# Kernel optimization log

Hardware: AMD Instinct MI355X
Metric: run time of the kernel (lower is better)

Reference implementation:

```python
import jax, jax.numpy as jnp
import numpy as np
from jax import lax

C = 768
SHIFT_DISTANCES = (1, 2, 3)


def _layernorm(x, g, b, eps=1e-5):
    m = jnp.mean(x, axis=-1, keepdims=True)
    v = jnp.mean((x - m) ** 2, axis=-1, keepdims=True)
    return (x - m) * lax.rsqrt(v + eps) * g + b


def setup_inputs() -> dict:
    key = jax.random.key(0)
    ks = jax.random.split(key, 16)
    B, T, N = 8, 16, 197
    inp = {
        "x": jax.random.normal(ks[0], (B * T, N, C), dtype=jnp.float32),
        "ln_g": jnp.ones((C,), jnp.float32),
        "ln_b": jnp.zeros((C,), jnp.float32),
        "gate_w": jax.random.normal(ks[1], (C, C), jnp.float32) * 0.02,
        "gate_b": jnp.zeros((C,), jnp.float32),
        "proj_w1": jax.random.normal(ks[2], (C, C), jnp.float32) * 0.02,
        "proj_b1": jnp.zeros((C,), jnp.float32),
        "proj_w2": jax.random.normal(ks[3], (C, C), jnp.float32) * 0.02,
        "proj_b2": jnp.zeros((C,), jnp.float32),
        "fusion_w": jnp.ones((len(SHIFT_DISTANCES),), jnp.float32),
        "num_frames": T,
    }
    for i, d in enumerate(SHIFT_DISTANCES):
        k = 2 * d + 1
        # depthwise Conv1d weight: (out=C, in/groups=1, k)
        inp[f"conv_w{i}"] = jax.random.normal(ks[4 + i], (C, 1, k), jnp.float32) * (1.0 / np.sqrt(k))
        inp[f"conv_b{i}"] = jnp.zeros((C,), jnp.float32)
    return inp


def _branch(x4, conv_w, conv_b, d, ln_g, ln_b, gate_w, gate_b):
    # x4: [B, T, N, C]
    B, T, N, Cc = x4.shape
    p = Cc // 3  # past / future split; static gets the remainder
    x_norm = jax.nn.relu(_layernorm(x4, ln_g, ln_b))
    # [B, T, N, C] -> [B*N, C, T] for depthwise conv over time
    x_1d = x_norm.transpose(0, 2, 3, 1).reshape(B * N, Cc, T)
    feat = lax.conv_general_dilated(
        x_1d, conv_w, window_strides=(1,), padding=[(d, d)],
        dimension_numbers=("NCH", "OIH", "NCH"), feature_group_count=Cc,
    ) + conv_b[None, :, None]
    feat = feat.reshape(B, N, Cc, T).transpose(0, 3, 1, 2)  # [B, T, N, C]
    gate = jax.nn.sigmoid(jnp.einsum("btnc,cd->btnd", feat, gate_w) + gate_b)
    y = gate * x4  # channelwise split-and-multiply fuses into one op
    y_past, y_future, y_static = y[..., :p], y[..., p:2 * p], y[..., 2 * p:]
    s = min(d, T)
    out_past = jnp.pad(y_past[:, s:], ((0, 0), (0, s), (0, 0), (0, 0)))  # lshift
    out_future = jnp.pad(y_future[:, :T - s], ((0, 0), (s, 0), (0, 0), (0, 0)))  # rshift
    return jnp.concatenate([out_past, out_future, y_static], axis=-1)


def reference(x, ln_g, ln_b, gate_w, gate_b, proj_w1, proj_b1, proj_w2, proj_b2,
              fusion_w, conv_w0, conv_b0, conv_w1, conv_b1, conv_w2, conv_b2,
              num_frames):
    B_T, N, Cc = x.shape
    T = num_frames
    B = B_T // T
    x4 = x.reshape(B, T, N, Cc)
    convs = [(conv_w0, conv_b0), (conv_w1, conv_b1), (conv_w2, conv_b2)]
    outs = jnp.stack([
        _branch(x4, cw, cb, d, ln_g, ln_b, gate_w, gate_b)
        for (cw, cb), d in zip(convs, SHIFT_DISTANCES)
    ], axis=0)  # [3, B, T, N, C]
    w = jax.nn.softmax(fusion_w)[:, None, None, None, None]
    fused = jnp.sum(w * outs, axis=0).reshape(B_T, N, Cc)
    h = jnp.einsum("bnc,cd->bnd", fused, proj_w1) + proj_b1
    h = jax.nn.gelu(h, approximate=False)
    h = jnp.einsum("bnc,cd->bnd", h, proj_w2) + proj_b2
    return x + h
```

## Files before the change

kernel.cpp:

```cpp
#include <hip/hip_runtime.h>
#include <math.h>


#define MROWS 25216
#define CD    768
#define NTOK  197
#define TFR   16

typedef __attribute__((ext_vector_type(8))) short short8;
typedef __attribute__((ext_vector_type(4))) float floatx4;
typedef unsigned int u32;

__device__ __forceinline__ unsigned short f2bf(float f) {
    union { float f; unsigned u; } v; v.f = f;
    unsigned r = v.u + 0x7FFFu + ((v.u >> 16) & 1u);
    return (unsigned short)(r >> 16);
}
__device__ __forceinline__ float bf2f(unsigned short h) {
    union { unsigned u; float f; } v; v.u = ((unsigned)h) << 16;
    return v.f;
}

__device__ __forceinline__ void gl2lds16(const void* g, void* l) {
    __builtin_amdgcn_global_load_lds(
        (__attribute__((address_space(1))) void*)(unsigned long long)g,
        (__attribute__((address_space(3))) void*)(u32)(unsigned long long)l,
        16, 0, 0);
}

__global__ __launch_bounds__(256)
void ln_relu_kernel(const float* __restrict__ x, const float* __restrict__ g,
                    const float* __restrict__ b, unsigned short* __restrict__ xn,
                    unsigned short* __restrict__ xb) {
    int row = blockIdx.x;
    int tid = threadIdx.x;
    const float* xr = x + (size_t)row * CD;
    float v0 = xr[tid], v1 = xr[tid + 256], v2 = xr[tid + 512];
    float s = v0 + v1 + v2;
    __shared__ float red[8];
#pragma unroll
    for (int off = 32; off; off >>= 1) s += __shfl_down(s, off, 64);
    int lane = tid & 63, w = tid >> 6;
    if (lane == 0) red[w] = s;
    __syncthreads();
    float mean = (red[0] + red[1] + red[2] + red[3]) * (1.0f / CD);
    float d0 = v0 - mean, d1 = v1 - mean, d2 = v2 - mean;
    float s2 = d0 * d0 + d1 * d1 + d2 * d2;
#pragma unroll
    for (int off = 32; off; off >>= 1) s2 += __shfl_down(s2, off, 64);
    if (lane == 0) red[4 + w] = s2;
    __syncthreads();
    float var = (red[4] + red[5] + red[6] + red[7]) * (1.0f / CD);
    float inv = rsqrtf(var + 1e-5f);
    unsigned short* xo = xn + (size_t)row * CD;
    unsigned short* xc = xb + (size_t)row * CD;
    float o0 = fmaxf(d0 * inv * g[tid]       + b[tid],       0.0f);
    float o1 = fmaxf(d1 * inv * g[tid + 256] + b[tid + 256], 0.0f);
    float o2 = fmaxf(d2 * inv * g[tid + 512] + b[tid + 512], 0.0f);
    xo[tid] = f2bf(o0); xo[tid + 256] = f2bf(o1); xo[tid + 512] = f2bf(o2);
    xc[tid] = f2bf(v0); xc[tid + 256] = f2bf(v1); xc[tid + 512] = f2bf(v2);
}

template <int D>
__device__ __forceinline__
void dw_body(const unsigned short* __restrict__ xn, const float* __restrict__ cw,
             const float* __restrict__ cb, unsigned short* __restrict__ feat) {
    constexpr int KK = 2 * D + 1;
    int gid = blockIdx.x * 256 + threadIdx.x;
    int bn = gid / 96;
    int cg = gid - bn * 96;
    int c0 = cg * 8;
    int b = bn / NTOK;
    size_t base = ((size_t)b * TFR * NTOK + (bn - b * NTOK)) * CD + c0;
    const size_t tstride = (size_t)NTOK * CD;

    short8 u[TFR];
#pragma unroll
    for (int t = 0; t < TFR; ++t)
        u[t] = *(const short8*)(xn + base + (size_t)t * tstride);

    float wgt[8][KK], bb[8];
#pragma unroll
    for (int q = 0; q < 8; ++q) {
        bb[q] = cb[c0 + q];
#pragma unroll
        for (int j = 0; j < KK; ++j) wgt[q][j] = cw[(c0 + q) * KK + j];
    }

#pragma unroll
    for (int t = 0; t < TFR; ++t) {
        float acc[8];
#pragma unroll
        for (int q = 0; q < 8; ++q) acc[q] = bb[q];
#pragma unroll
        for (int j = 0; j < KK; ++j) {
            int tj = t + j - D;
            if (tj < 0 || tj >= TFR) continue;
#pragma unroll
            for (int q = 0; q < 8; ++q)
                acc[q] += bf2f((unsigned short)u[tj][q]) * wgt[q][j];
        }
        short8 o;
#pragma unroll
        for (int q = 0; q < 8; ++q) o[q] = (short)f2bf(acc[q]);
        *(short8*)(feat + base + (size_t)t * tstride) = o;
    }
}

__global__ __launch_bounds__(256)
void dwconv_all(const unsigned short* __restrict__ xn,
                const float* __restrict__ cw0, const float* __restrict__ cb0,
                const float* __restrict__ cw1, const float* __restrict__ cb1,
                const float* __restrict__ cw2, const float* __restrict__ cb2,
                unsigned short* __restrict__ f1, unsigned short* __restrict__ f2,
                unsigned short* __restrict__ f3) {
    if (blockIdx.y == 0)      dw_body<1>(xn, cw0, cb0, f1);
    else if (blockIdx.y == 1) dw_body<2>(xn, cw1, cb1, f2);
    else                      dw_body<3>(xn, cw2, cb2, f3);
}

__global__ __launch_bounds__(256)
void wprep3_kernel(const float* __restrict__ w0, const float* __restrict__ w1,
                   const float* __restrict__ w2, unsigned short* __restrict__ t0,
                   unsigned short* __restrict__ t1, unsigned short* __restrict__ t2) {
    const float* w = blockIdx.y == 0 ? w0 : blockIdx.y == 1 ? w1 : w2;
    unsigned short* wt = blockIdx.y == 0 ? t0 : blockIdx.y == 1 ? t1 : t2;
    int gid = blockIdx.x * 256 + threadIdx.x;
    int n = gid / CD, k = gid - n * CD;
    wt[gid] = f2bf(w[(size_t)k * CD + n]);
}

__global__ __launch_bounds__(256)
void fuse_kernel(const unsigned short* __restrict__ y1,
                 const unsigned short* __restrict__ y2,
                 const unsigned short* __restrict__ y3,
                 unsigned short* __restrict__ fused) {
    int gid = blockIdx.x * 256 + threadIdx.x;
    int m = gid / 96;
    int kk = (gid - m * 96) * 8;
    int t = (m / NTOK) & 15;
    float vals[8] = {0.f, 0.f, 0.f, 0.f, 0.f, 0.f, 0.f, 0.f};
    const unsigned short* ys[3] = {y1, y2, y3};
#pragma unroll
    for (int d = 1; d <= 3; ++d) {
        int src; bool ok;
        if (kk < 256)      { src = m + d * NTOK; ok = (t + d) < TFR; }
        else if (kk < 512) { src = m - d * NTOK; ok = (t - d) >= 0; }
        else               { src = m;            ok = true; }
        if (ok) {
            short8 u = *(const short8*)(ys[d - 1] + (size_t)src * CD + kk);
#pragma unroll
            for (int e = 0; e < 8; ++e) vals[e] += bf2f((unsigned short)u[e]);
        }
    }
    short8 o;
#pragma unroll
    for (int e = 0; e < 8; ++e) o[e] = (short)f2bf(vals[e]);
    *(short8*)(fused + (size_t)m * CD + kk) = o;
}

template <int EPI>
__global__ __launch_bounds__(512)
void gemm_kernel(const unsigned short* __restrict__ A,
                 const unsigned short* __restrict__ Bt,
                 const float* __restrict__ bias,
                 const unsigned short* __restrict__ xb,
                 const float* __restrict__ xf,
                 float* __restrict__ outf,
                 unsigned short* __restrict__ outh0,
                 unsigned short* __restrict__ outh1,
                 unsigned short* __restrict__ outh2,
                 const float* __restrict__ fw) {
    extern __shared__ __align__(16) char smem[];
    int tid  = threadIdx.x;
    int m0   = blockIdx.x * 128;
    int n0   = blockIdx.y * 256;
    int wave = tid >> 6, lane = tid & 63;
    int wr   = wave >> 2, wc = wave & 3;
    int quad = lane >> 4, l16 = lane & 15;
    int rr   = lane >> 3;
    int ckx  = ((lane & 7) ^ rr) * 8;

    floatx4 acc[4][4];
#pragma unroll
    for (int i = 0; i < 4; ++i)
#pragma unroll
        for (int j = 0; j < 4; ++j) acc[i][j] = (floatx4){0.f, 0.f, 0.f, 0.f};

    auto Asb = [&](int bb) { return (unsigned short*)(smem + bb * 16384); };
    auto Bsb = [&](int bb) { return (unsigned short*)(smem + 49152 + bb * 32768); };

    auto sA = [&](int t, int bb, int h) {
        int q = wave + h * 8;
        gl2lds16(A + (size_t)(m0 + q * 8 + rr) * CD + t * 64 + ckx, Asb(bb) + q * 512);
    };
    auto sB = [&](int t, int bb, int h) {
        int q = wave + h * 8;
        gl2lds16(Bt + (size_t)(n0 + q * 8 + rr) * CD + t * 64 + ckx, Bsb(bb) + q * 512);
    };
    auto ldA = [&](int bb, int i, int kk) -> short8 {
        int r = wr * 64 + i * 16 + l16;
        int slot = (kk * 4 + quad) ^ (l16 & 7);
        return *(const short8*)((const char*)Asb(bb) + r * 128 + slot * 16);
    };
    auto ldB = [&](int bb, int j, int kk) -> short8 {
        int r = wc * 64 + j * 16 + l16;
        int slot = (kk * 4 + quad) ^ (l16 & 7);
        return *(const short8*)((const char*)Bsb(bb) + r * 128 + slot * 16);
    };

#define LGKM0 do { asm volatile("s_waitcnt lgkmcnt(0)" ::: "memory"); \
                   __builtin_amdgcn_sched_barrier(0); } while (0)
#define PBAR  do { __builtin_amdgcn_s_barrier(); \
                   __builtin_amdgcn_sched_barrier(0); } while (0)

    auto kstep = [&](int t, bool doStage) {
        int bb = t % 3, bn = (t + 2) % 3;
        short8 a0[4], a1[4], u, v;
#pragma unroll
        for (int i = 0; i < 4; ++i) a0[i] = ldA(bb, i, 0);
        u = ldB(bb, 0, 0); v = ldB(bb, 1, 0);
        if (doStage) { sA(t + 2, bn, 0); sA(t + 2, bn, 1); }
        LGKM0;
        __builtin_amdgcn_s_setprio(1);
#pragma unroll
        for (int i = 0; i < 4; ++i) {
            acc[i][0] = __builtin_amdgcn_mfma_f32_16x16x32_bf16(a0[i], u, acc[i][0], 0, 0, 0);
            acc[i][1] = __builtin_amdgcn_mfma_f32_16x16x32_bf16(a0[i], v, acc[i][1], 0, 0, 0);
        }
        __builtin_amdgcn_s_setprio(0);
        PBAR;
        u = ldB(bb, 2, 0); v = ldB(bb, 3, 0);
        if (doStage) { sB(t + 2, bn, 0); sB(t + 2, bn, 1); }
        LGKM0;
        __builtin_amdgcn_s_setprio(1);
#pragma unroll
        for (int i = 0; i < 4; ++i) {
            acc[i][2] = __builtin_amdgcn_mfma_f32_16x16x32_bf16(a0[i], u, acc[i][2], 0, 0, 0);
            acc[i][3] = __builtin_amdgcn_mfma_f32_16x16x32_bf16(a0[i], v, acc[i][3], 0, 0, 0);
        }
        __builtin_amdgcn_s_setprio(0);
        PBAR;
#pragma unroll
        for (int i = 0; i < 4; ++i) a1[i] = ldA(bb, i, 1);
        u = ldB(bb, 0, 1); v = ldB(bb, 1, 1);
        if (doStage) { sB(t + 2, bn, 2); sB(t + 2, bn, 3); }
        LGKM0;
        __builtin_amdgcn_s_setprio(1);
#pragma unroll
        for (int i = 0; i < 4; ++i) {
            acc[i][0] = __builtin_amdgcn_mfma_f32_16x16x32_bf16(a1[i], u, acc[i][0], 0, 0, 0);
            acc[i][1] = __builtin_amdgcn_mfma_f32_16x16x32_bf16(a1[i], v, acc[i][1], 0, 0, 0);
        }
        __builtin_amdgcn_s_setprio(0);
        PBAR;
        u = ldB(bb, 2, 1); v = ldB(bb, 3, 1);
        LGKM0;
        __builtin_amdgcn_s_setprio(1);
#pragma unroll
        for (int i = 0; i < 4; ++i) {
            acc[i][2] = __builtin_amdgcn_mfma_f32_16x16x32_bf16(a1[i], u, acc[i][2], 0, 0, 0);
            acc[i][3] = __builtin_amdgcn_mfma_f32_16x16x32_bf16(a1[i], v, acc[i][3], 0, 0, 0);
        }
        __builtin_amdgcn_s_setprio(0);
    };

    constexpr int NT = CD / 64;
    sA(0, 0, 0); sA(0, 0, 1); sB(0, 0, 0); sB(0, 0, 1); sB(0, 0, 2); sB(0, 0, 3);
    sA(1, 1, 0); sA(1, 1, 1); sB(1, 1, 0); sB(1, 1, 1); sB(1, 1, 2); sB(1, 1, 3);
    for (int t = 0; t < NT - 1; ++t) {
        asm volatile("s_waitcnt vmcnt(6)" ::: "memory");
        PBAR;
        kstep(t, t + 2 < NT);
    }
    asm volatile("s_waitcnt vmcnt(0)" ::: "memory");
    PBAR;
    kstep(NT - 1, false);

    float wd = 0.f;
    int widx = (EPI == 0) ? (blockIdx.x / 197) : 0;
    unsigned short* outh = outh0;
    if (EPI == 0) {
        float f0 = fw[0], f1 = fw[1], f2 = fw[2];
        float mx = fmaxf(f0, fmaxf(f1, f2));
        float e0 = expf(f0 - mx), e1 = expf(f1 - mx), e2 = expf(f2 - mx);
        float inv = 1.f / (e0 + e1 + e2);
        wd = (widx == 0 ? e0 : widx == 1 ? e1 : e2) * inv;
        outh = widx == 0 ? outh0 : widx == 1 ? outh1 : outh2;
    }

    float (*fE)[268] = (float (*)[268])smem;
    __syncthreads();
#pragma unroll
    for (int j = 0; j < 4; ++j) {
        int col = wc * 64 + j * 16 + l16;
        float bc = bias[n0 + col];
#pragma unroll
        for (int i = 0; i < 4; ++i)
#pragma unroll
            for (int r = 0; r < 4; ++r)
                fE[wr * 64 + i * 16 + quad * 4 + r][col] = acc[i][j][r] + bc;
    }
    __syncthreads();
#pragma unroll
    for (int it = 0; it < 8; ++it) {
        int lr = it * 16 + (tid >> 5);
        int cg = tid & 31;
        size_t lrow = (size_t)(m0 + lr) - (size_t)widx * MROWS;
        int gcol = n0 + cg * 8;
        size_t idx = lrow * CD + gcol;
        floatx4 v0 = *(const floatx4*)&fE[lr][cg * 8];
        floatx4 v1 = *(const floatx4*)&fE[lr][cg * 8 + 4];
        if (EPI == 0) {
            short8 xv = *(const short8*)(xb + idx);
            short8 o;
#pragma unroll
            for (int e = 0; e < 8; ++e) {
                float vv = e < 4 ? v0[e] : v1[e - 4];
                float gte = 1.f / (1.f + expf(-vv));
                o[e] = (short)f2bf(wd * gte * bf2f((unsigned short)xv[e]));
            }
            *(short8*)(outh + idx) = o;
        } else if (EPI == 1) {
            short8 o;
#pragma unroll
            for (int e = 0; e < 8; ++e) {
                float vv = e < 4 ? v0[e] : v1[e - 4];
                float gl = 0.5f * vv * (1.0f + erff(vv * 0.70710678118f));
                o[e] = (short)f2bf(gl);
            }
            *(short8*)(outh + idx) = o;
        } else {
            floatx4 x0 = *(const floatx4*)(xf + idx);
            floatx4 x1 = *(const floatx4*)(xf + idx + 4);
#pragma unroll
            for (int e = 0; e < 4; ++e) { v0[e] += x0[e]; v1[e] += x1[e]; }
            *(floatx4*)(outf + idx)     = v0;
            *(floatx4*)(outf + idx + 4) = v1;
        }
    }
#undef LGKM0
#undef PBAR
}

extern "C" void kernel_launch(void* const* d_in, const int* in_sizes, int n_in,
                              void* d_out, int out_size, void* d_ws, size_t ws_size,
                              hipStream_t stream) {
    const float* x      = (const float*)d_in[0];
    const float* ln_g   = (const float*)d_in[1];
    const float* ln_b   = (const float*)d_in[2];
    const float* gate_w = (const float*)d_in[3];
    const float* gate_b = (const float*)d_in[4];
    const float* pw1    = (const float*)d_in[5];
    const float* pb1    = (const float*)d_in[6];
    const float* pw2    = (const float*)d_in[7];
    const float* pb2    = (const float*)d_in[8];
    const float* fw     = (const float*)d_in[9];
    const float* cw[3]  = {(const float*)d_in[11], (const float*)d_in[13], (const float*)d_in[15]};
    const float* cb[3]  = {(const float*)d_in[12], (const float*)d_in[14], (const float*)d_in[16]};

    char* ws = (char*)d_ws;
    const size_t SB = (size_t)MROWS * CD * 2;
    unsigned short* gwt  = (unsigned short*)(ws + 0);
    unsigned short* p1t  = (unsigned short*)(ws + 1179648);
    unsigned short* p2t  = (unsigned short*)(ws + 2359296);
    unsigned short* xn   = (unsigned short*)(ws + 3538944);
    unsigned short* xb   = (unsigned short*)(ws + 3538944 + SB);
    unsigned short* f1   = (unsigned short*)(ws + 3538944 + 2 * SB);
    unsigned short* f2   = (unsigned short*)(ws + 3538944 + 3 * SB);
    unsigned short* f3   = (unsigned short*)(ws + 3538944 + 4 * SB);
    unsigned short* y2s  = (unsigned short*)(ws + 3538944 + 5 * SB);
    unsigned short* y3s  = (unsigned short*)(ws + 3538944 + 6 * SB);
    unsigned short* y1    = xn;
    unsigned short* fused = f3;
    unsigned short* h1    = xn;

    const int LDSB = 147456;
    hipFuncSetAttribute(reinterpret_cast<const void*>(gemm_kernel<0>),
                        hipFuncAttributeMaxDynamicSharedMemorySize, LDSB);
    hipFuncSetAttribute(reinterpret_cast<const void*>(gemm_kernel<1>),
                        hipFuncAttributeMaxDynamicSharedMemorySize, LDSB);
    hipFuncSetAttribute(reinterpret_cast<const void*>(gemm_kernel<2>),
                        hipFuncAttributeMaxDynamicSharedMemorySize, LDSB);

    dim3 wg(2304, 3);
    wprep3_kernel<<<wg, 256, 0, stream>>>(gate_w, pw1, pw2, gwt, p1t, p2t);
    ln_relu_kernel<<<MROWS, 256, 0, stream>>>(x, ln_g, ln_b, xn, xb);

    dim3 dg(591, 3);
    dwconv_all<<<dg, 256, 0, stream>>>(xn, cw[0], cb[0], cw[1], cb[1], cw[2], cb[2],
                                       f1, f2, f3);

    dim3 gg3(591, 3);
    gemm_kernel<0><<<gg3, 512, LDSB, stream>>>(f1, gwt, gate_b, xb, nullptr,
                                               nullptr, y1, y2s, y3s, fw);

    fuse_kernel<<<9456, 256, 0, stream>>>(y1, y2s, y3s, fused);

    dim3 gg(197, 3);
    gemm_kernel<1><<<gg, 512, LDSB, stream>>>(fused, p1t, pb1, nullptr, nullptr,
                                              nullptr, h1, nullptr, nullptr, nullptr);
    gemm_kernel<2><<<gg, 512, LDSB, stream>>>(h1, p2t, pb2, nullptr, x,
                                              (float*)d_out, nullptr, nullptr, nullptr, nullptr);
}
```

Measured before the change: 529.2 us.

## Fuse layernorm into depthwise conv and shrink GEMM K-tile for higher occupancy

Merges the layernorm+ReLU kernel with the three depthwise temporal convolutions, so each block handles one (batch, token) column across all frames. This removes the bf16 normalized intermediate and its extra global round trip. The GEMM K-step drops from 64 to 32, cutting LDS from 147KB to 72KB with a new swizzle, and launch bounds now request more resident blocks. The epilogue is staged in two halves to fit the smaller LDS, and expf is swapped for __expf. The tradeoffs are more K iterations and barriers in the GEMM and only 192 threads per conv block.

```diff
diff --git a/kernel.cpp b/kernel.cpp
--- a/kernel.cpp
+++ b/kernel.cpp
@@ -8,6 +8,7 @@
 #define TFR   16
 
 typedef __attribute__((ext_vector_type(8))) short short8;
+typedef __attribute__((ext_vector_type(4))) short short4v;
 typedef __attribute__((ext_vector_type(4))) float floatx4;
 typedef unsigned int u32;
 
@@ -28,95 +29,105 @@
         16, 0, 0);
 }
 
-__global__ __launch_bounds__(256)
-void ln_relu_kernel(const float* __restrict__ x, const float* __restrict__ g,
-                    const float* __restrict__ b, unsigned short* __restrict__ xn,
-                    unsigned short* __restrict__ xb) {
-    int row = blockIdx.x;
-    int tid = threadIdx.x;
-    const float* xr = x + (size_t)row * CD;
-    float v0 = xr[tid], v1 = xr[tid + 256], v2 = xr[tid + 512];
-    float s = v0 + v1 + v2;
-    __shared__ float red[8];
-#pragma unroll
-    for (int off = 32; off; off >>= 1) s += __shfl_down(s, off, 64);
-    int lane = tid & 63, w = tid >> 6;
-    if (lane == 0) red[w] = s;
-    __syncthreads();
-    float mean = (red[0] + red[1] + red[2] + red[3]) * (1.0f / CD);
-    float d0 = v0 - mean, d1 = v1 - mean, d2 = v2 - mean;
-    float s2 = d0 * d0 + d1 * d1 + d2 * d2;
-#pragma unroll
-    for (int off = 32; off; off >>= 1) s2 += __shfl_down(s2, off, 64);
-    if (lane == 0) red[4 + w] = s2;
-    __syncthreads();
-    float var = (red[4] + red[5] + red[6] + red[7]) * (1.0f / CD);
-    float inv = rsqrtf(var + 1e-5f);
-    unsigned short* xo = xn + (size_t)row * CD;
-    unsigned short* xc = xb + (size_t)row * CD;
-    float o0 = fmaxf(d0 * inv * g[tid]       + b[tid],       0.0f);
-    float o1 = fmaxf(d1 * inv * g[tid + 256] + b[tid + 256], 0.0f);
-    float o2 = fmaxf(d2 * inv * g[tid + 512] + b[tid + 512], 0.0f);
-    xo[tid] = f2bf(o0); xo[tid + 256] = f2bf(o1); xo[tid + 512] = f2bf(o2);
-    xc[tid] = f2bf(v0); xc[tid + 256] = f2bf(v1); xc[tid + 512] = f2bf(v2);
-}
-
 template <int D>
 __device__ __forceinline__
-void dw_body(const unsigned short* __restrict__ xn, const float* __restrict__ cw,
-             const float* __restrict__ cb, unsigned short* __restrict__ feat) {
+void dw_store(const float (&xn)[TFR][4], const float* __restrict__ cw,
+              const float* __restrict__ cb, unsigned short* __restrict__ f,
+              size_t base, size_t tstr, int c0) {
     constexpr int KK = 2 * D + 1;
-    int gid = blockIdx.x * 256 + threadIdx.x;
-    int bn = gid / 96;
-    int cg = gid - bn * 96;
-    int c0 = cg * 8;
-    int b = bn / NTOK;
-    size_t base = ((size_t)b * TFR * NTOK + (bn - b * NTOK)) * CD + c0;
-    const size_t tstride = (size_t)NTOK * CD;
-
-    short8 u[TFR];
-#pragma unroll
-    for (int t = 0; t < TFR; ++t)
-        u[t] = *(const short8*)(xn + base + (size_t)t * tstride);
-
-    float wgt[8][KK], bb[8];
-#pragma unroll
-    for (int q = 0; q < 8; ++q) {
-        bb[q] = cb[c0 + q];
-#pragma unroll
-        for (int j = 0; j < KK; ++j) wgt[q][j] = cw[(c0 + q) * KK + j];
-    }
-
-#pragma unroll
-    for (int t = 0; t < TFR; ++t) {
-        float acc[8];
-#pragma unroll
-        for (int q = 0; q < 8; ++q) acc[q] = bb[q];
+    float wj[4][KK], cbv[4];
+#pragma unroll
+    for (int q = 0; q < 4; ++q) {
+        cbv[q] = cb[c0 + q];
+#pragma unroll
+        for (int j = 0; j < KK; ++j) wj[q][j] = cw[(c0 + q) * KK + j];
+    }
+#pragma unroll
+    for (int t = 0; t < TFR; ++t) {
+        float acc[4] = {cbv[0], cbv[1], cbv[2], cbv[3]};
 #pragma unroll
         for (int j = 0; j < KK; ++j) {
             int tj = t + j - D;
             if (tj < 0 || tj >= TFR) continue;
 #pragma unroll
-            for (int q = 0; q < 8; ++q)
-                acc[q] += bf2f((unsigned short)u[tj][q]) * wgt[q][j];
-        }
-        short8 o;
-#pragma unroll
-        for (int q = 0; q < 8; ++q) o[q] = (short)f2bf(acc[q]);
-        *(short8*)(feat + base + (size_t)t * tstride) = o;
-    }
-}
-
-__global__ __launch_bounds__(256)
-void dwconv_all(const unsigned short* __restrict__ xn,
-                const float* __restrict__ cw0, const float* __restrict__ cb0,
-                const float* __restrict__ cw1, const float* __restrict__ cb1,
-                const float* __restrict__ cw2, const float* __restrict__ cb2,
-                unsigned short* __restrict__ f1, unsigned short* __restrict__ f2,
-                unsigned short* __restrict__ f3) {
-    if (blockIdx.y == 0)      dw_body<1>(xn, cw0, cb0, f1);
-    else if (blockIdx.y == 1) dw_body<2>(xn, cw1, cb1, f2);
-    else                      dw_body<3>(xn, cw2, cb2, f3);
+            for (int q = 0; q < 4; ++q) acc[q] += xn[tj][q] * wj[q][j];
+        }
+        short4v o;
+#pragma unroll
+        for (int q = 0; q < 4; ++q) o[q] = (short)f2bf(acc[q]);
+        *(short4v*)(f + base + t * tstr) = o;
+    }
+}
+
+__global__ __launch_bounds__(192)
+void ln_dw_kernel(const float* __restrict__ x, const float* __restrict__ g,
+                  const float* __restrict__ bia,
+                  const float* __restrict__ cw0, const float* __restrict__ cb0,
+                  const float* __restrict__ cw1, const float* __restrict__ cb1,
+                  const float* __restrict__ cw2, const float* __restrict__ cb2,
+                  unsigned short* __restrict__ xb,
+                  unsigned short* __restrict__ f1,
+                  unsigned short* __restrict__ f2,
+                  unsigned short* __restrict__ f3) {
+    int blk = blockIdx.x, tid = threadIdx.x;
+    int b = blk / NTOK, n = blk - b * NTOK;
+    int c0 = tid * 4;
+    size_t base = ((size_t)b * TFR * NTOK + n) * CD + c0;
+    const size_t tstr = (size_t)NTOK * CD;
+    int lane = tid & 63, w = tid >> 6;
+
+    float xn[TFR][4];
+    float ps[TFR];
+#pragma unroll
+    for (int t = 0; t < TFR; ++t) {
+        float4 xv = *(const float4*)(x + base + t * tstr);
+        xn[t][0] = xv.x; xn[t][1] = xv.y; xn[t][2] = xv.z; xn[t][3] = xv.w;
+        ps[t] = xv.x + xv.y + xv.z + xv.w;
+        short4v o; o[0] = (short)f2bf(xv.x); o[1] = (short)f2bf(xv.y);
+        o[2] = (short)f2bf(xv.z); o[3] = (short)f2bf(xv.w);
+        *(short4v*)(xb + base + t * tstr) = o;
+    }
+    __shared__ float red[TFR][4];
+#pragma unroll
+    for (int t = 0; t < TFR; ++t) {
+        float v = ps[t];
+#pragma unroll
+        for (int off = 32; off; off >>= 1) v += __shfl_down(v, off, 64);
+        if (lane == 0) red[t][w] = v;
+    }
+    __syncthreads();
+    float mean[TFR];
+#pragma unroll
+    for (int t = 0; t < TFR; ++t) mean[t] = (red[t][0] + red[t][1] + red[t][2]) * (1.0f / CD);
+    __syncthreads();
+#pragma unroll
+    for (int t = 0; t < TFR; ++t) {
+        float d0 = xn[t][0] - mean[t], d1 = xn[t][1] - mean[t];
+        float d2 = xn[t][2] - mean[t], d3 = xn[t][3] - mean[t];
+        ps[t] = d0 * d0 + d1 * d1 + d2 * d2 + d3 * d3;
+    }
+#pragma unroll
+    for (int t = 0; t < TFR; ++t) {
+        float v = ps[t];
+#pragma unroll
+        for (int off = 32; off; off >>= 1) v += __shfl_down(v, off, 64);
+        if (lane == 0) red[t][w] = v;
+    }
+    __syncthreads();
+    float gv[4], bv[4];
+#pragma unroll
+    for (int q = 0; q < 4; ++q) { gv[q] = g[c0 + q]; bv[q] = bia[c0 + q]; }
+#pragma unroll
+    for (int t = 0; t < TFR; ++t) {
+        float var = (red[t][0] + red[t][1] + red[t][2]) * (1.0f / CD);
+        float inv = rsqrtf(var + 1e-5f);
+#pragma unroll
+        for (int q = 0; q < 4; ++q)
+            xn[t][q] = fmaxf((xn[t][q] - mean[t]) * inv * gv[q] + bv[q], 0.0f);
+    }
+    dw_store<1>(xn, cw0, cb0, f1, base, tstr, c0);
+    dw_store<2>(xn, cw1, cb1, f2, base, tstr, c0);
+    dw_store<3>(xn, cw2, cb2, f3, base, tstr, c0);
 }
 
 __global__ __launch_bounds__(256)
@@ -160,7 +171,7 @@
 }
 
 template <int EPI>
-__global__ __launch_bounds__(512)
+__global__ __launch_bounds__(512, 4)
 void gemm_kernel(const unsigned short* __restrict__ A,
                  const unsigned short* __restrict__ Bt,
                  const float* __restrict__ bias,
@@ -178,8 +189,9 @@
     int wave = tid >> 6, lane = tid & 63;
     int wr   = wave >> 2, wc = wave & 3;
     int quad = lane >> 4, l16 = lane & 15;
-    int rr   = lane >> 3;
-    int ckx  = ((lane & 7) ^ rr) * 8;
+    int r4   = lane >> 2;
+    int ckx  = (((lane & 3) ^ ((lane >> 3) & 3)) * 8);
+    int rdsl = (quad ^ ((l16 >> 1) & 3)) * 16;
 
     floatx4 acc[4][4];
 #pragma unroll
@@ -187,26 +199,22 @@
 #pragma unroll
         for (int j = 0; j < 4; ++j) acc[i][j] = (floatx4){0.f, 0.f, 0.f, 0.f};
 
-    auto Asb = [&](int bb) { return (unsigned short*)(smem + bb * 16384); };
-    auto Bsb = [&](int bb) { return (unsigned short*)(smem + 49152 + bb * 32768); };
-
-    auto sA = [&](int t, int bb, int h) {
-        int q = wave + h * 8;
-        gl2lds16(A + (size_t)(m0 + q * 8 + rr) * CD + t * 64 + ckx, Asb(bb) + q * 512);
+    auto Asb = [&](int bb) { return smem + bb * 8192; };
+    auto Bsb = [&](int bb) { return smem + 24576 + bb * 16384; };
+
+    const size_t aoff = (size_t)(m0 + wave * 16 + r4) * CD + ckx;
+    const size_t boff = (size_t)(n0 + wave * 16 + r4) * CD + ckx;
+    auto sA = [&](int t, int bb) {
+        gl2lds16(A + aoff + t * 32, Asb(bb) + wave * 1024);
     };
     auto sB = [&](int t, int bb, int h) {
-        int q = wave + h * 8;
-        gl2lds16(Bt + (size_t)(n0 + q * 8 + rr) * CD + t * 64 + ckx, Bsb(bb) + q * 512);
-    };
-    auto ldA = [&](int bb, int i, int kk) -> short8 {
-        int r = wr * 64 + i * 16 + l16;
-        int slot = (kk * 4 + quad) ^ (l16 & 7);
-        return *(const short8*)((const char*)Asb(bb) + r * 128 + slot * 16);
-    };
-    auto ldB = [&](int bb, int j, int kk) -> short8 {
-        int r = wc * 64 + j * 16 + l16;
-        int slot = (kk * 4 + quad) ^ (l16 & 7);
-        return *(const short8*)((const char*)Bsb(bb) + r * 128 + slot * 16);
+        gl2lds16(Bt + boff + (size_t)h * 128 * CD + t * 32, Bsb(bb) + (wave + h * 8) * 1024);
+    };
+    auto ldA = [&](int bb, int i) -> short8 {
+        return *(const short8*)(Asb(bb) + (wr * 64 + i * 16 + l16) * 64 + rdsl);
+    };
+    auto ldB = [&](int bb, int j) -> short8 {
+        return *(const short8*)(Bsb(bb) + (wc * 64 + j * 16 + l16) * 64 + rdsl);
     };
 
 #define LGKM0 do { asm volatile("s_waitcnt lgkmcnt(0)" ::: "memory"); \
@@ -215,61 +223,38 @@
                    __builtin_amdgcn_sched_barrier(0); } while (0)
 
     auto kstep = [&](int t, bool doStage) {
-        int bb = t % 3, bn = (t + 2) % 3;
-        short8 a0[4], a1[4], u, v;
-#pragma unroll
-        for (int i = 0; i < 4; ++i) a0[i] = ldA(bb, i, 0);
-        u = ldB(bb, 0, 0); v = ldB(bb, 1, 0);
-        if (doStage) { sA(t + 2, bn, 0); sA(t + 2, bn, 1); }
+        int bb = t % 3, bnx = (t + 2) % 3;
+        short8 a[4], u, v;
+#pragma unroll
+        for (int i = 0; i < 4; ++i) a[i] = ldA(bb, i);
+        u = ldB(bb, 0); v = ldB(bb, 1);
+        if (doStage) { sA(t + 2, bnx); sB(t + 2, bnx, 0); }
         LGKM0;
         __builtin_amdgcn_s_setprio(1);
 #pragma unroll
         for (int i = 0; i < 4; ++i) {
-            acc[i][0] = __builtin_amdgcn_mfma_f32_16x16x32_bf16(a0[i], u, acc[i][0], 0, 0, 0);
-            acc[i][1] = __builtin_amdgcn_mfma_f32_16x16x32_bf16(a0[i], v, acc[i][1], 0, 0, 0);
+            acc[i][0] = __builtin_amdgcn_mfma_f32_16x16x32_bf16(a[i], u, acc[i][0], 0, 0, 0);
+            acc[i][1] = __builtin_amdgcn_mfma_f32_16x16x32_bf16(a[i], v, acc[i][1], 0, 0, 0);
         }
         __builtin_amdgcn_s_setprio(0);
         PBAR;
-        u = ldB(bb, 2, 0); v = ldB(bb, 3, 0);
-        if (doStage) { sB(t + 2, bn, 0); sB(t + 2, bn, 1); }
+        u = ldB(bb, 2); v = ldB(bb, 3);
+        if (doStage) sB(t + 2, bnx, 1);
         LGKM0;
         __builtin_amdgcn_s_setprio(1);
 #pragma unroll
         for (int i = 0; i < 4; ++i) {
-            acc[i][2] = __builtin_amdgcn_mfma_f32_16x16x32_bf16(a0[i], u, acc[i][2], 0, 0, 0);
-            acc[i][3] = __builtin_amdgcn_mfma_f32_16x16x32_bf16(a0[i], v, acc[i][3], 0, 0, 0);
+            acc[i][2] = __builtin_amdgcn_mfma_f32_16x16x32_bf16(a[i], u, acc[i][2], 0, 0, 0);
+            acc[i][3] = __builtin_amdgcn_mfma_f32_16x16x32_bf16(a[i], v, acc[i][3], 0, 0, 0);
         }
         __builtin_amdgcn_s_setprio(0);
-        PBAR;
-#pragma unroll
-        for (int i = 0; i < 4; ++i) a1[i] = ldA(bb, i, 1);
-        u = ldB(bb, 0, 1); v = ldB(bb, 1, 1);
-        if (doStage) { sB(t + 2, bn, 2); sB(t + 2, bn, 3); }
-        LGKM0;
-        __builtin_amdgcn_s_setprio(1);
-#pragma unroll
-        for (int i = 0; i < 4; ++i) {
-            acc[i][0] = __builtin_amdgcn_mfma_f32_16x16x32_bf16(a1[i], u, acc[i][0], 0, 0, 0);
-            acc[i][1] = __builtin_amdgcn_mfma_f32_16x16x32_bf16(a1[i], v, acc[i][1], 0, 0, 0);
-        }
-        __builtin_amdgcn_s_setprio(0);
-        PBAR;
-        u = ldB(bb, 2, 1); v = ldB(bb, 3, 1);
-        LGKM0;
-        __builtin_amdgcn_s_setprio(1);
-#pragma unroll
-        for (int i = 0; i < 4; ++i) {
-            acc[i][2] = __builtin_amdgcn_mfma_f32_16x16x32_bf16(a1[i], u, acc[i][2], 0, 0, 0);
-            acc[i][3] = __builtin_amdgcn_mfma_f32_16x16x32_bf16(a1[i], v, acc[i][3], 0, 0, 0);
-        }
-        __builtin_amdgcn_s_setprio(0);
-    };
-
-    constexpr int NT = CD / 64;
-    sA(0, 0, 0); sA(0, 0, 1); sB(0, 0, 0); sB(0, 0, 1); sB(0, 0, 2); sB(0, 0, 3);
-    sA(1, 1, 0); sA(1, 1, 1); sB(1, 1, 0); sB(1, 1, 1); sB(1, 1, 2); sB(1, 1, 3);
+    };
+
+    constexpr int NT = CD / 32;
+    sA(0, 0); sB(0, 0, 0); sB(0, 0, 1);
+    sA(1, 1); sB(1, 1, 0); sB(1, 1, 1);
     for (int t = 0; t < NT - 1; ++t) {
-        asm volatile("s_waitcnt vmcnt(6)" ::: "memory");
+        asm volatile("s_waitcnt vmcnt(3)" ::: "memory");
         PBAR;
         kstep(t, t + 2 < NT);
     }
@@ -283,60 +268,64 @@
     if (EPI == 0) {
         float f0 = fw[0], f1 = fw[1], f2 = fw[2];
         float mx = fmaxf(f0, fmaxf(f1, f2));
-        float e0 = expf(f0 - mx), e1 = expf(f1 - mx), e2 = expf(f2 - mx);
+        float e0 = __expf(f0 - mx), e1 = __expf(f1 - mx), e2 = __expf(f2 - mx);
         float inv = 1.f / (e0 + e1 + e2);
         wd = (widx == 0 ? e0 : widx == 1 ? e1 : e2) * inv;
         outh = widx == 0 ? outh0 : widx == 1 ? outh1 : outh2;
     }
 
-    float (*fE)[268] = (float (*)[268])smem;
-    __syncthreads();
-#pragma unroll
-    for (int j = 0; j < 4; ++j) {
-        int col = wc * 64 + j * 16 + l16;
-        float bc = bias[n0 + col];
-#pragma unroll
-        for (int i = 0; i < 4; ++i)
-#pragma unroll
-            for (int r = 0; r < 4; ++r)
-                fE[wr * 64 + i * 16 + quad * 4 + r][col] = acc[i][j][r] + bc;
-    }
-    __syncthreads();
-#pragma unroll
-    for (int it = 0; it < 8; ++it) {
-        int lr = it * 16 + (tid >> 5);
-        int cg = tid & 31;
-        size_t lrow = (size_t)(m0 + lr) - (size_t)widx * MROWS;
-        int gcol = n0 + cg * 8;
-        size_t idx = lrow * CD + gcol;
-        floatx4 v0 = *(const floatx4*)&fE[lr][cg * 8];
-        floatx4 v1 = *(const floatx4*)&fE[lr][cg * 8 + 4];
-        if (EPI == 0) {
-            short8 xv = *(const short8*)(xb + idx);
-            short8 o;
-#pragma unroll
-            for (int e = 0; e < 8; ++e) {
-                float vv = e < 4 ? v0[e] : v1[e - 4];
-                float gte = 1.f / (1.f + expf(-vv));
-                o[e] = (short)f2bf(wd * gte * bf2f((unsigned short)xv[e]));
+    float (*fE)[264] = (float (*)[264])smem;
+#pragma unroll
+    for (int p = 0; p < 2; ++p) {
+        __syncthreads();
+        if (wr == p) {
+#pragma unroll
+            for (int j = 0; j < 4; ++j) {
+                int col = wc * 64 + j * 16 + l16;
+                float bc = bias[n0 + col];
+#pragma unroll
+                for (int i = 0; i < 4; ++i)
+#pragma unroll
+                    for (int r = 0; r < 4; ++r)
+                        fE[i * 16 + quad * 4 + r][col] = acc[i][j][r] + bc;
             }
-            *(short8*)(outh + idx) = o;
-        } else if (EPI == 1) {
-            short8 o;
-#pragma unroll
-            for (int e = 0; e < 8; ++e) {
-                float vv = e < 4 ? v0[e] : v1[e - 4];
-                float gl = 0.5f * vv * (1.0f + erff(vv * 0.70710678118f));
-                o[e] = (short)f2bf(gl);
+        }
+        __syncthreads();
+#pragma unroll
+        for (int it = 0; it < 4; ++it) {
+            int lr = it * 16 + (tid >> 5);
+            int cg = tid & 31;
+            size_t lrow = (size_t)(m0 + p * 64 + lr) - (size_t)widx * MROWS;
+            size_t idx = lrow * CD + n0 + cg * 8;
+            floatx4 v0 = *(const floatx4*)&fE[lr][cg * 8];
+            floatx4 v1 = *(const floatx4*)&fE[lr][cg * 8 + 4];
+            if (EPI == 0) {
+                short8 xv = *(const short8*)(xb + idx);
+                short8 o;
+#pragma unroll
+                for (int e = 0; e < 8; ++e) {
+                    float vv = e < 4 ? v0[e] : v1[e - 4];
+                    float gte = 1.f / (1.f + __expf(-vv));
+                    o[e] = (short)f2bf(wd * gte * bf2f((unsigned short)xv[e]));
+                }
+                *(short8*)(outh + idx) = o;
+            } else if (EPI == 1) {
+                short8 o;
+#pragma unroll
+                for (int e = 0; e < 8; ++e) {
+                    float vv = e < 4 ? v0[e] : v1[e - 4];
+                    float gl = 0.5f * vv * (1.0f + erff(vv * 0.70710678118f));
+                    o[e] = (short)f2bf(gl);
+                }
+                *(short8*)(outh + idx) = o;
+            } else {
+                floatx4 x0 = *(const floatx4*)(xf + idx);
+                floatx4 x1 = *(const floatx4*)(xf + idx + 4);
+#pragma unroll
+                for (int e = 0; e < 4; ++e) { v0[e] += x0[e]; v1[e] += x1[e]; }
+                *(floatx4*)(outf + idx)     = v0;
+                *(floatx4*)(outf + idx + 4) = v1;
             }
-            *(short8*)(outh + idx) = o;
-        } else {
-            floatx4 x0 = *(const floatx4*)(xf + idx);
-            floatx4 x1 = *(const floatx4*)(xf + idx + 4);
-#pragma unroll
-            for (int e = 0; e < 4; ++e) { v0[e] += x0[e]; v1[e] += x1[e]; }
-            *(floatx4*)(outf + idx)     = v0;
-            *(floatx4*)(outf + idx + 4) = v1;
         }
     }
 #undef LGKM0
@@ -364,18 +353,17 @@
     unsigned short* gwt  = (unsigned short*)(ws + 0);
     unsigned short* p1t  = (unsigned short*)(ws + 1179648);
     unsigned short* p2t  = (unsigned short*)(ws + 2359296);
-    unsigned short* xn   = (unsigned short*)(ws + 3538944);
+    unsigned short* y1   = (unsigned short*)(ws + 3538944);
     unsigned short* xb   = (unsigned short*)(ws + 3538944 + SB);
     unsigned short* f1   = (unsigned short*)(ws + 3538944 + 2 * SB);
     unsigned short* f2   = (unsigned short*)(ws + 3538944 + 3 * SB);
     unsigned short* f3   = (unsigned short*)(ws + 3538944 + 4 * SB);
     unsigned short* y2s  = (unsigned short*)(ws + 3538944 + 5 * SB);
     unsigned short* y3s  = (unsigned short*)(ws + 3538944 + 6 * SB);
-    unsigned short* y1    = xn;
     unsigned short* fused = f3;
-    unsigned short* h1    = xn;
-
-    const int LDSB = 147456;
+    unsigned short* h1    = y1;
+
+    const int LDSB = 73728;
     hipFuncSetAttribute(reinterpret_cast<const void*>(gemm_kernel<0>),
                         hipFuncAttributeMaxDynamicSharedMemorySize, LDSB);
     hipFuncSetAttribute(reinterpret_cast<const void*>(gemm_kernel<1>),
@@ -385,11 +373,10 @@
 
     dim3 wg(2304, 3);
     wprep3_kernel<<<wg, 256, 0, stream>>>(gate_w, pw1, pw2, gwt, p1t, p2t);
-    ln_relu_kernel<<<MROWS, 256, 0, stream>>>(x, ln_g, ln_b, xn, xb);
-
-    dim3 dg(591, 3);
-    dwconv_all<<<dg, 256, 0, stream>>>(xn, cw[0], cb[0], cw[1], cb[1], cw[2], cb[2],
-                                       f1, f2, f3);
+
+    ln_dw_kernel<<<8 * NTOK, 192, 0, stream>>>(x, ln_g, ln_b,
+                                               cw[0], cb[0], cw[1], cb[1], cw[2], cb[2],
+                                               xb, f1, f2, f3);
 
     dim3 gg3(591, 3);
     gemm_kernel<0><<<gg3, 512, LDSB, stream>>>(f1, gwt, gate_b, xb, nullptr,
```

Measured after the change: 485.8 us. -8.2%, faster.
